# Kernel optimization log

Hardware: AMD Instinct MI355X
Metric: run time of the kernel (lower is better)

Reference implementation:

```python
import jax, jax.numpy as jnp
import numpy as np

N_NODES = 100000
D_IN = 128
D_OUT = 128
N_EDGES = 1600000
BN_EPS = 1e-5


def _glorot(key, fan_in, fan_out):
    limit = np.sqrt(6.0 / (fan_in + fan_out))
    return jax.random.uniform(key, (fan_in, fan_out), jnp.float32, -limit, limit)


def setup_inputs() -> dict:
    key = jax.random.key(0)
    k_x, k_e, k0, k1, k2 = jax.random.split(key, 5)
    x = jax.random.normal(k_x, (N_NODES, D_IN), jnp.float32)
    edge_index = jax.random.randint(k_e, (2, N_EDGES), 0, N_NODES, jnp.int64)
    return {
        "x": x,
        "edge_index": edge_index,
        "kernel": _glorot(k0, D_IN, D_OUT),
        "kernel1": _glorot(k1, D_IN, D_IN),
        "kernel2": _glorot(k2, D_IN, D_IN),
        "gamma": jnp.ones((D_IN,), jnp.float32),
        "beta": jnp.zeros((D_IN,), jnp.float32),
    }


def reference(x, edge_index, kernel, kernel1, kernel2, gamma, beta):
    N = x.shape[0]
    # BatchNorm1d (training mode: batch statistics, biased variance)
    mean = jnp.mean(x, axis=0)
    var = jnp.var(x, axis=0)
    xn = (x - mean) * jax.lax.rsqrt(var + BN_EPS) * gamma + beta

    mapped = xn @ kernel                                  # [N, D_OUT]
    s1 = jnp.tanh(jnp.sum((xn @ kernel1) * xn, axis=1))   # [N]
    s2 = jnp.tanh(jnp.sum((xn @ kernel2) * xn, axis=1))   # [N]

    src, dst = edge_index[0], edge_index[1]
    # edge score: adj values are 1 -> leaky_relu(s1[i] + s2[j]) for edge (i,j)
    e = jax.nn.leaky_relu(s1[src] + s2[dst], negative_slope=0.01)  # [E]

    # sparse row-wise softmax over dim 1 (segment softmax over src)
    emax = jax.ops.segment_max(e, src, num_segments=N)
    emax = jnp.where(jnp.isfinite(emax), emax, 0.0)
    ee = jnp.exp(e - emax[src])
    denom = jax.ops.segment_sum(ee, src, num_segments=N)
    attn = ee / jnp.maximum(denom[src], 1e-16)            # [E]

    # attention_adj @ mapped_inputs (scatter-add over src rows)
    out = jax.ops.segment_sum(attn[:, None] * mapped[dst], src, num_segments=N)
    return jax.nn.relu(out)
```

## Files before the change

kernel.cpp:

```cpp
#include <hip/hip_runtime.h>
#include <math.h>

#define N_NODES 100000
#define D 128
#define N_EDGES 1600000
#define BN_EPS 1e-5f
#define SCAN_NB 200
#define SCAN_BC 500
#define EG_BLOCKS 1563
#define EH_BLOCKS 782
#define GEMM_BLOCKS 1563

typedef __attribute__((ext_vector_type(8))) short bf16x8;
typedef __attribute__((ext_vector_type(4))) float f32x4;

__device__ inline unsigned short f2bf(float f) {
    unsigned int u = __float_as_uint(f);
    unsigned int r = u + 0x7FFFu + ((u >> 16) & 1u);
    return (unsigned short)(r >> 16);
}
__device__ inline float bf2f(unsigned short b) {
    return __uint_as_float(((unsigned int)b) << 16);
}

__global__ __launch_bounds__(256)
void stats_hist(const float* __restrict__ x, float* __restrict__ sums,
                const int* __restrict__ src, int* __restrict__ cnt,
                int* __restrict__ rank) {
    if (blockIdx.x < 256) {
        const int col  = threadIdx.x & 127;
        const int half = threadIdx.x >> 7;
        float s = 0.f, sq = 0.f;
        for (int r = blockIdx.x * 2 + half; r < N_NODES; r += 512) {
            float v = x[(size_t)r * D + col];
            s += v; sq += v * v;
        }
        __shared__ float ls[2][128];
        __shared__ float lq[2][128];
        ls[half][col] = s; lq[half][col] = sq;
        __syncthreads();
        if (threadIdx.x < 128) {
            atomicAdd(&sums[col],       ls[0][col] + ls[1][col]);
            atomicAdd(&sums[128 + col], lq[0][col] + lq[1][col]);
        }
    } else {
        const int b = blockIdx.x - 256;
        int* c = cnt + (size_t)(b & 7) * N_NODES;
        const int base = b * 2048 + threadIdx.x;
        if (b < EH_BLOCKS - 1) {
            int s[8];
#pragma unroll
            for (int j = 0; j < 8; ++j) s[j] = src[base + j * 256];
            int r[8];
#pragma unroll
            for (int j = 0; j < 8; ++j) r[j] = atomicAdd(&c[s[j]], 1);
#pragma unroll
            for (int j = 0; j < 8; ++j) rank[base + j * 256] = r[j];
        } else {
#pragma unroll
            for (int j = 0; j < 8; ++j) {
                int i = base + j * 256;
                if (i < N_EDGES) rank[i] = atomicAdd(&c[src[i]], 1);
            }
        }
    }
}

__global__ __launch_bounds__(256)
void finalize_pack(const float* __restrict__ sums, const float* __restrict__ gamma,
                   const float* __restrict__ beta, float* __restrict__ scale,
                   float* __restrict__ bias,
                   const float* __restrict__ k0, const float* __restrict__ k1,
                   const float* __restrict__ k2, unsigned short* __restrict__ wpack) {
    if (blockIdx.x == 0) {
        if (threadIdx.x < 128) {
            int c = threadIdx.x;
            float mean = sums[c] * (1.0f / N_NODES);
            float var  = sums[128 + c] * (1.0f / N_NODES) - mean * mean;
            float rstd = rsqrtf(var + BN_EPS);
            float sc = gamma[c] * rstd;
            scale[c] = sc;
            bias[c]  = beta[c] - mean * sc;
        }
        return;
    }
    int idx = (blockIdx.x - 1) * 256 + threadIdx.x;
    if (idx >= 3 * 4 * 8 * 64) return;
    int m    = idx >> 11;
    int r    = idx & 2047;
    int kk   = r >> 9;
    int r2   = r & 511;
    int nt   = r2 >> 6;
    int lane = r2 & 63;
    const float* W = (m == 0) ? k0 : (m == 1) ? k1 : k2;
    int col   = nt * 16 + (lane & 15);
    int kbase = kk * 32 + (lane >> 4) * 8;
    unsigned int wh[4], wl[4];
#pragma unroll
    for (int i = 0; i < 4; ++i) {
        float a = W[(kbase + 2 * i)     * 128 + col];
        float b = W[(kbase + 2 * i + 1) * 128 + col];
        unsigned short ah = f2bf(a), bh = f2bf(b);
        unsigned short al = f2bf(a - bf2f(ah)), bl = f2bf(b - bf2f(bh));
        wh[i] = (unsigned int)ah | ((unsigned int)bh << 16);
        wl[i] = (unsigned int)al | ((unsigned int)bl << 16);
    }
    uint4* outp = (uint4*)wpack;
    outp[idx]        = make_uint4(wh[0], wh[1], wh[2], wh[3]);
    outp[6144 + idx] = make_uint4(wl[0], wl[1], wl[2], wl[3]);
}

__global__ __launch_bounds__(256)
void scan_blocksum(const int* __restrict__ cnt, int* __restrict__ bsum) {
    __shared__ int red[256];
    const int b = blockIdx.x, t = threadIdx.x;
    const int base = b * SCAN_BC;
    int s = 0;
    for (int i = t; i < SCAN_BC; i += 256) {
        int node = base + i;
#pragma unroll
        for (int x = 0; x < 8; ++x) s += cnt[(size_t)x * N_NODES + node];
    }
    red[t] = s;
    __syncthreads();
    for (int off = 128; off; off >>= 1) {
        if (t < off) red[t] += red[t + off];
        __syncthreads();
    }
    if (t == 0) bsum[b] = red[0];
}

__global__ __launch_bounds__(256)
void scan_bases(int* __restrict__ bsum, int* __restrict__ row_off) {
    __shared__ int v[256];
    const int t = threadIdx.x;
    v[t] = (t < SCAN_NB) ? bsum[t] : 0;
    __syncthreads();
    for (int off = 1; off < 256; off <<= 1) {
        int u = (t >= off) ? v[t - off] : 0;
        __syncthreads();
        v[t] += u;
        __syncthreads();
    }
    if (t < SCAN_NB) bsum[t] = (t == 0) ? 0 : v[t - 1];
    if (t == 0) row_off[N_NODES] = v[SCAN_NB - 1];
}

__global__ __launch_bounds__(256)
void scan_write(int* __restrict__ cnt, const int* __restrict__ bsum,
                int* __restrict__ row_off) {
    __shared__ int tsum[256];
    const int b = blockIdx.x, t = threadIdx.x;
    const int i0 = b * SCAN_BC + t * 2;
    int c0[8], c1[8];
    int tot0 = 0, tot1 = 0;
    if (t < 250) {
#pragma unroll
        for (int x = 0; x < 8; ++x) {
            c0[x] = cnt[(size_t)x * N_NODES + i0];
            c1[x] = cnt[(size_t)x * N_NODES + i0 + 1];
            tot0 += c0[x]; tot1 += c1[x];
        }
    }
    tsum[t] = tot0 + tot1;
    __syncthreads();
    for (int off = 1; off < 256; off <<= 1) {
        int u = (t >= off) ? tsum[t - off] : 0;
        __syncthreads();
        tsum[t] += u;
        __syncthreads();
    }
    if (t < 250) {
        int run = bsum[b] + ((t == 0) ? 0 : tsum[t - 1]);
        row_off[i0] = run;
        int acc = run;
#pragma unroll
        for (int x = 0; x < 8; ++x) { cnt[(size_t)x * N_NODES + i0] = acc; acc += c0[x]; }
        run += tot0;
        row_off[i0 + 1] = run;
        acc = run;
#pragma unroll
        for (int x = 0; x < 8; ++x) { cnt[(size_t)x * N_NODES + i0 + 1] = acc; acc += c1[x]; }
    }
}

__global__ __launch_bounds__(256, 4)
void gemm_scatter(const float* __restrict__ x, const unsigned short* __restrict__ wpack,
                  const float* __restrict__ scale, const float* __restrict__ bias,
                  unsigned short* __restrict__ mapped, float* __restrict__ s1,
                  float* __restrict__ s2,
                  const int* __restrict__ src, const int* __restrict__ dst,
                  const int* __restrict__ cnt, const int* __restrict__ rank,
                  int* __restrict__ dst_sorted) {
    __shared__ unsigned short xbuf[64 * 128];
    if (blockIdx.x >= GEMM_BLOCKS) {
        const int b = blockIdx.x - GEMM_BLOCKS;
        const int* c = cnt + (size_t)((b >> 1) & 7) * N_NODES;
        const int base = b * 1024 + threadIdx.x;
#pragma unroll
        for (int k = 0; k < 4; ++k) {
            int i = base + k * 256;
            if (i < N_EDGES) dst_sorted[c[src[i]] + rank[i]] = dst[i];
        }
        return;
    }
    const int tid  = threadIdx.x;
    const int wave = tid >> 6, lane = tid & 63;
    const int base = blockIdx.x * 64;
    char* xb = (char*)xbuf;

    float2 sc = ((const float2*)scale)[lane];
    float2 bs = ((const float2*)bias)[lane];

    unsigned int hipack[16];
#pragma unroll
    for (int rr = 0; rr < 16; ++rr) {
        int row  = wave * 16 + rr;
        int node = base + row;
        float2 v = make_float2(0.f, 0.f);
        if (node < N_NODES) v = ((const float2*)x)[(size_t)node * 64 + lane];
        float f0 = v.x * sc.x + bs.x;
        float f1 = v.y * sc.y + bs.y;
        unsigned short h0 = f2bf(f0), h1 = f2bf(f1);
        unsigned short l0 = f2bf(f0 - bf2f(h0)), l1 = f2bf(f1 - bf2f(h1));
        hipack[rr] = (unsigned int)h0 | ((unsigned int)h1 << 16);
        int byte = (row * 256 + lane * 4) ^ ((row & 7) << 4);
        *(unsigned int*)(xb + byte) = (unsigned int)l0 | ((unsigned int)l1 << 16);
    }
    __syncthreads();

    const int arow  = wave * 16 + (lane & 15);
    const int lrow0 = wave * 16 + (lane >> 4) * 4;

    bf16x8 al[4];
#pragma unroll
    for (int kk = 0; kk < 4; ++kk) {
        int byte = (arow * 256 + kk * 64 + (lane >> 4) * 16) ^ ((arow & 7) << 4);
        al[kk] = *(const bf16x8*)(xb + byte);
    }
    unsigned int xlo[16];
#pragma unroll
    for (int nt = 0; nt < 8; ++nt) {
#pragma unroll
        for (int reg = 0; reg < 4; ++reg) {
            int lrow = lrow0 + reg;
            int col  = nt * 16 + (lane & 15);
            int byte = (lrow * 256 + col * 2) ^ ((lrow & 7) << 4);
            unsigned short v = *(const unsigned short*)(xb + byte);
            int idx = nt * 4 + reg;
            if (idx & 1) xlo[idx >> 1] |= ((unsigned int)v) << 16;
            else         xlo[idx >> 1]  = v;
        }
    }
    __syncthreads();

#pragma unroll
    for (int rr = 0; rr < 16; ++rr) {
        int row  = wave * 16 + rr;
        int byte = (row * 256 + lane * 4) ^ ((row & 7) << 4);
        *(unsigned int*)(xb + byte) = hipack[rr];
    }
    __syncthreads();

    bf16x8 ah[4];
#pragma unroll
    for (int kk = 0; kk < 4; ++kk) {
        int byte = (arow * 256 + kk * 64 + (lane >> 4) * 16) ^ ((arow & 7) << 4);
        ah[kk] = *(const bf16x8*)(xb + byte);
    }

    const bf16x8* wp = (const bf16x8*)wpack;

    {
        f32x4 acc[8] = {};
#pragma unroll
        for (int kk = 0; kk < 4; ++kk) {
#pragma unroll
            for (int nt = 0; nt < 8; ++nt) {
                bf16x8 b = wp[(kk * 8 + nt) * 64 + lane];
                acc[nt] = __builtin_amdgcn_mfma_f32_16x16x32_bf16(ah[kk], b, acc[nt], 0, 0, 0);
            }
        }
        int crow = base + wave * 16 + (lane >> 4) * 4;
        int ccol = lane & 15;
#pragma unroll
        for (int nt = 0; nt < 8; ++nt) {
#pragma unroll
            for (int reg = 0; reg < 4; ++reg) {
                int node = crow + reg;
                if (node < N_NODES)
                    mapped[(size_t)node * 128 + nt * 16 + ccol] = f2bf(acc[nt][reg]);
            }
        }
    }

    {
        float p1[4] = {0.f, 0.f, 0.f, 0.f};
        float p2[4] = {0.f, 0.f, 0.f, 0.f};
#pragma unroll
        for (int nt = 0; nt < 8; ++nt) {
            f32x4 a1 = {0.f, 0.f, 0.f, 0.f};
            f32x4 a2 = {0.f, 0.f, 0.f, 0.f};
#pragma unroll
            for (int kk = 0; kk < 4; ++kk) {
                int fi = (kk * 8 + nt) * 64 + lane;
                bf16x8 b1h = wp[2048 * 1 + fi];
                bf16x8 b1l = wp[6144 + 2048 * 1 + fi];
                bf16x8 b2h = wp[2048 * 2 + fi];
                bf16x8 b2l = wp[6144 + 2048 * 2 + fi];
                a1 = __builtin_amdgcn_mfma_f32_16x16x32_bf16(ah[kk], b1h, a1, 0, 0, 0);
                a1 = __builtin_amdgcn_mfma_f32_16x16x32_bf16(al[kk], b1h, a1, 0, 0, 0);
                a1 = __builtin_amdgcn_mfma_f32_16x16x32_bf16(ah[kk], b1l, a1, 0, 0, 0);
                a2 = __builtin_amdgcn_mfma_f32_16x16x32_bf16(ah[kk], b2h, a2, 0, 0, 0);
                a2 = __builtin_amdgcn_mfma_f32_16x16x32_bf16(al[kk], b2h, a2, 0, 0, 0);
                a2 = __builtin_amdgcn_mfma_f32_16x16x32_bf16(ah[kk], b2l, a2, 0, 0, 0);
            }
            int col = nt * 16 + (lane & 15);
#pragma unroll
            for (int reg = 0; reg < 4; ++reg) {
                int lrow = lrow0 + reg;
                int byte = (lrow * 256 + col * 2) ^ ((lrow & 7) << 4);
                float xh = bf2f(*(const unsigned short*)(xb + byte));
                int idx = nt * 4 + reg;
                unsigned short lo16 = (idx & 1) ? (unsigned short)(xlo[idx >> 1] >> 16)
                                                : (unsigned short)(xlo[idx >> 1] & 0xFFFFu);
                float xv = xh + bf2f(lo16);
                p1[reg] = fmaf(a1[reg], xv, p1[reg]);
                p2[reg] = fmaf(a2[reg], xv, p2[reg]);
            }
        }
#pragma unroll
        for (int reg = 0; reg < 4; ++reg) {
#pragma unroll
            for (int off = 1; off < 16; off <<= 1) {
                p1[reg] += __shfl_xor(p1[reg], off);
                p2[reg] += __shfl_xor(p2[reg], off);
            }
        }
        if ((lane & 15) == 0) {
            int nbase = base + wave * 16 + (lane >> 4) * 4;
#pragma unroll
            for (int reg = 0; reg < 4; ++reg) {
                int node = nbase + reg;
                if (node < N_NODES) {
                    s1[node] = tanhf(p1[reg]);
                    s2[node] = tanhf(p2[reg]);
                }
            }
        }
    }
}

__global__ __launch_bounds__(256)
void node_aggregate(const int* __restrict__ row_off, const int* __restrict__ dst_sorted,
                    const float* __restrict__ s1, const float* __restrict__ s2,
                    const unsigned int* __restrict__ mapped,
                    float* __restrict__ out) {
    const int wave = threadIdx.x >> 6, lane = threadIdx.x & 63;
    const int n = blockIdx.x * 4 + wave;
    if (n >= N_NODES) return;
    const int beg = row_off[n], end = row_off[n + 1];
    const int deg = end - beg;
    float acc0 = 0.f, acc1 = 0.f, den = 0.f;

#define GATHER8(WSRC, DSRC, J)                                                   \
    {                                                                            \
        float w0 = __shfl(WSRC, (J) + 0), w1 = __shfl(WSRC, (J) + 1);            \
        float w2 = __shfl(WSRC, (J) + 2), w3 = __shfl(WSRC, (J) + 3);            \
        float w4 = __shfl(WSRC, (J) + 4), w5 = __shfl(WSRC, (J) + 5);            \
        float w6 = __shfl(WSRC, (J) + 6), w7 = __shfl(WSRC, (J) + 7);            \
        int d0 = __shfl(DSRC, (J) + 0), d1 = __shfl(DSRC, (J) + 1);              \
        int d2 = __shfl(DSRC, (J) + 2), d3 = __shfl(DSRC, (J) + 3);              \
        int d4 = __shfl(DSRC, (J) + 4), d5 = __shfl(DSRC, (J) + 5);              \
        int d6 = __shfl(DSRC, (J) + 6), d7 = __shfl(DSRC, (J) + 7);              \
        unsigned int m0 = mapped[(size_t)d0 * 64 + lane];                        \
        unsigned int m1 = mapped[(size_t)d1 * 64 + lane];                        \
        unsigned int m2 = mapped[(size_t)d2 * 64 + lane];                        \
        unsigned int m3 = mapped[(size_t)d3 * 64 + lane];                        \
        unsigned int m4 = mapped[(size_t)d4 * 64 + lane];                        \
        unsigned int m5 = mapped[(size_t)d5 * 64 + lane];                        \
        unsigned int m6 = mapped[(size_t)d6 * 64 + lane];                        \
        unsigned int m7 = mapped[(size_t)d7 * 64 + lane];                        \
        acc0 = fmaf(w0, bf2f((unsigned short)(m0 & 0xFFFFu)), acc0);             \
        acc1 = fmaf(w0, bf2f((unsigned short)(m0 >> 16)), acc1);                 \
        acc0 = fmaf(w1, bf2f((unsigned short)(m1 & 0xFFFFu)), acc0);             \
        acc1 = fmaf(w1, bf2f((unsigned short)(m1 >> 16)), acc1);                 \
        acc0 = fmaf(w2, bf2f((unsigned short)(m2 & 0xFFFFu)), acc0);             \
        acc1 = fmaf(w2, bf2f((unsigned short)(m2 >> 16)), acc1);                 \
        acc0 = fmaf(w3, bf2f((unsigned short)(m3 & 0xFFFFu)), acc0);             \
        acc1 = fmaf(w3, bf2f((unsigned short)(m3 >> 16)), acc1);                 \
        acc0 = fmaf(w4, bf2f((unsigned short)(m4 & 0xFFFFu)), acc0);             \
        acc1 = fmaf(w4, bf2f((unsigned short)(m4 >> 16)), acc1);                 \
        acc0 = fmaf(w5, bf2f((unsigned short)(m5 & 0xFFFFu)), acc0);             \
        acc1 = fmaf(w5, bf2f((unsigned short)(m5 >> 16)), acc1);                 \
        acc0 = fmaf(w6, bf2f((unsigned short)(m6 & 0xFFFFu)), acc0);             \
        acc1 = fmaf(w6, bf2f((unsigned short)(m6 >> 16)), acc1);                 \
        acc0 = fmaf(w7, bf2f((unsigned short)(m7 & 0xFFFFu)), acc0);             \
        acc1 = fmaf(w7, bf2f((unsigned short)(m7 >> 16)), acc1);                 \
    }

    if (deg > 0 && deg <= 64) {
        float s1n = s1[n];
        int   d_l = 0; float e_l = -INFINITY;
        if (lane < deg) {
            d_l = dst_sorted[beg + lane];
            float v = s1n + s2[d_l];
            e_l = v > 0.f ? v : 0.01f * v;
        }
        float m = e_l;
#pragma unroll
        for (int off = 1; off < 64; off <<= 1) m = fmaxf(m, __shfl_xor(m, off));
        float w_l = (lane < deg) ? expf(e_l - m) : 0.f;
        den = w_l;
        int j = 0;
        for (; j + 8 <= deg; j += 8) GATHER8(w_l, d_l, j)
        for (; j < deg; ++j) {
            float wj = __shfl(w_l, j);
            int   dj = __shfl(d_l, j);
            unsigned int mv = mapped[(size_t)dj * 64 + lane];
            acc0 = fmaf(wj, bf2f((unsigned short)(mv & 0xFFFFu)), acc0);
            acc1 = fmaf(wj, bf2f((unsigned short)(mv >> 16)), acc1);
        }
    } else if (deg > 64) {
        float s1n = s1[n];
        float m = -INFINITY;
        for (int chunk = beg; chunk < end; chunk += 64) {
            if (chunk + lane < end) {
                int dj = dst_sorted[chunk + lane];
                float v = s1n + s2[dj];
                m = fmaxf(m, v > 0.f ? v : 0.01f * v);
            }
        }
#pragma unroll
        for (int off = 1; off < 64; off <<= 1) m = fmaxf(m, __shfl_xor(m, off));
        for (int chunk = beg; chunk < end; chunk += 64) {
            int nc = min(64, end - chunk);
            int   d_l = 0; float w_l = 0.f;
            if (lane < nc) {
                d_l = dst_sorted[chunk + lane];
                float v = s1n + s2[d_l];
                float e = v > 0.f ? v : 0.01f * v;
                w_l = expf(e - m);
            }
            den += w_l;
            int j = 0;
            for (; j + 8 <= nc; j += 8) GATHER8(w_l, d_l, j)
            for (; j < nc; ++j) {
                float wj = __shfl(w_l, j);
                int   dj = __shfl(d_l, j);
                unsigned int mv = mapped[(size_t)dj * 64 + lane];
                acc0 = fmaf(wj, bf2f((unsigned short)(mv & 0xFFFFu)), acc0);
                acc1 = fmaf(wj, bf2f((unsigned short)(mv >> 16)), acc1);
            }
        }
    }
#undef GATHER8

    if (deg > 0) {
#pragma unroll
        for (int off = 1; off < 64; off <<= 1) den += __shfl_xor(den, off);
        float inv = 1.f / fmaxf(den, 1e-16f);
        acc0 *= inv; acc1 *= inv;
    }
    ((float2*)out)[(size_t)n * 64 + lane] = make_float2(fmaxf(acc0, 0.f), fmaxf(acc1, 0.f));
}

extern "C" void kernel_launch(void* const* d_in, const int* in_sizes, int n_in,
                              void* d_out, int out_size, void* d_ws, size_t ws_size,
                              hipStream_t stream) {
    const float* x     = (const float*)d_in[0];
    const int*   ei    = (const int*)d_in[1];
    const float* k0    = (const float*)d_in[2];
    const float* k1    = (const float*)d_in[3];
    const float* k2    = (const float*)d_in[4];
    const float* gamma = (const float*)d_in[5];
    const float* beta  = (const float*)d_in[6];
    float* out = (float*)d_out;

    const int* src = ei;
    const int* dst = ei + N_EDGES;

    char* ws = (char*)d_ws;
    unsigned short* wpack = (unsigned short*)ws;           ws += 6 * 128 * 128 * 2;
    float* s1       = (float*)ws;                          ws += N_NODES * 4;
    float* s2       = (float*)ws;                          ws += N_NODES * 4;
    float* scale    = (float*)ws;                          ws += 128 * 4;
    float* bias     = (float*)ws;                          ws += 128 * 4;
    float* sums     = (float*)ws;                          ws += 256 * 4;
    int*   bsum     = (int*)ws;                            ws += 256 * 4;
    int*   row_off  = (int*)ws;                            ws += (N_NODES + 1) * 4;
    int*   cnt      = (int*)ws;                            ws += (size_t)8 * N_NODES * 4;
    int*   rank     = (int*)ws;                            ws += (size_t)N_EDGES * 4;
    int*   dst_sorted = (int*)ws;                          ws += (size_t)N_EDGES * 4;
    unsigned short* mapped = (unsigned short*)ws;          ws += (size_t)N_NODES * D * 2;

    hipMemsetAsync(sums, 0, 256 * sizeof(float), stream);
    hipMemsetAsync(cnt, 0, (size_t)8 * N_NODES * sizeof(int), stream);

    stats_hist<<<256 + EH_BLOCKS, 256, 0, stream>>>(x, sums, src, cnt, rank);
    finalize_pack<<<25, 256, 0, stream>>>(sums, gamma, beta, scale, bias,
                                          k0, k1, k2, wpack);
    scan_blocksum<<<SCAN_NB, 256, 0, stream>>>(cnt, bsum);
    scan_bases<<<1, 256, 0, stream>>>(bsum, row_off);
    scan_write<<<SCAN_NB, 256, 0, stream>>>(cnt, bsum, row_off);
    gemm_scatter<<<GEMM_BLOCKS + EG_BLOCKS, 256, 0, stream>>>(
        x, wpack, scale, bias, mapped, s1, s2, src, dst, cnt, rank, dst_sorted);
    node_aggregate<<<(N_NODES + 3) / 4, 256, 0, stream>>>(row_off, dst_sorted,
                                                          s1, s2,
                                                          (const unsigned int*)mapped,
                                                          out);
}
```

Before: 308.2 us.

## Spread edge histogram across stats, pack and GEMM launches; widen gather unroll

The src-degree histogram windows are split across three kernels (stats, finalize_pack, and the GEMM launch) so the atomic histogram work overlaps with BN statistics, weight packing and the dense GEMM, instead of mostly running alongside the stats pass. The edge scatter into dst_sorted moves out of the GEMM launch into its own kernel after the scan, which adds a launch but leaves the GEMM kernel free to host histogram blocks. Separately, node_aggregate gathers 16 neighbour rows per batch before falling back to 8, to keep more loads in flight. The risks are the extra launch, register pressure from the wider gather, and an unbalanced split that leaves one kernel as the bottleneck.

```diff
diff --git a/kernel.cpp b/kernel.cpp
--- a/kernel.cpp
+++ b/kernel.cpp
@@ -9,6 +9,9 @@
 #define SCAN_BC 500
 #define EG_BLOCKS 1563
 #define EH_BLOCKS 782
+#define H1 156
+#define H2 16
+#define H3 (EH_BLOCKS - H1 - H2)
 #define GEMM_BLOCKS 1563
 
 typedef __attribute__((ext_vector_type(8))) short bf16x8;
@@ -21,6 +24,28 @@
 }
 __device__ inline float bf2f(unsigned short b) {
     return __uint_as_float(((unsigned int)b) << 16);
+}
+
+__device__ inline void hist_window(int w, const int* __restrict__ src,
+                                   int* __restrict__ cnt, int* __restrict__ rank) {
+    int* c = cnt + (size_t)(w & 7) * N_NODES;
+    const int base = w * 2048 + threadIdx.x;
+    if (w < EH_BLOCKS - 1) {
+        int s[8];
+#pragma unroll
+        for (int j = 0; j < 8; ++j) s[j] = src[base + j * 256];
+        int r[8];
+#pragma unroll
+        for (int j = 0; j < 8; ++j) r[j] = atomicAdd(&c[s[j]], 1);
+#pragma unroll
+        for (int j = 0; j < 8; ++j) rank[base + j * 256] = r[j];
+    } else {
+#pragma unroll
+        for (int j = 0; j < 8; ++j) {
+            int i = base + j * 256;
+            if (i < N_EDGES) rank[i] = atomicAdd(&c[src[i]], 1);
+        }
+    }
 }
 
 __global__ __launch_bounds__(256)
@@ -44,25 +69,7 @@
             atomicAdd(&sums[128 + col], lq[0][col] + lq[1][col]);
         }
     } else {
-        const int b = blockIdx.x - 256;
-        int* c = cnt + (size_t)(b & 7) * N_NODES;
-        const int base = b * 2048 + threadIdx.x;
-        if (b < EH_BLOCKS - 1) {
-            int s[8];
-#pragma unroll
-            for (int j = 0; j < 8; ++j) s[j] = src[base + j * 256];
-            int r[8];
-#pragma unroll
-            for (int j = 0; j < 8; ++j) r[j] = atomicAdd(&c[s[j]], 1);
-#pragma unroll
-            for (int j = 0; j < 8; ++j) rank[base + j * 256] = r[j];
-        } else {
-#pragma unroll
-            for (int j = 0; j < 8; ++j) {
-                int i = base + j * 256;
-                if (i < N_EDGES) rank[i] = atomicAdd(&c[src[i]], 1);
-            }
-        }
+        hist_window(blockIdx.x - 256, src, cnt, rank);
     }
 }
 
@@ -71,7 +78,13 @@
                    const float* __restrict__ beta, float* __restrict__ scale,
                    float* __restrict__ bias,
                    const float* __restrict__ k0, const float* __restrict__ k1,
-                   const float* __restrict__ k2, unsigned short* __restrict__ wpack) {
+                   const float* __restrict__ k2, unsigned short* __restrict__ wpack,
+                   const int* __restrict__ src, int* __restrict__ cnt,
+                   int* __restrict__ rank) {
+    if (blockIdx.x >= 25) {
+        hist_window(H1 + (blockIdx.x - 25), src, cnt, rank);
+        return;
+    }
     if (blockIdx.x == 0) {
         if (threadIdx.x < 128) {
             int c = threadIdx.x;
@@ -110,98 +123,16 @@
     outp[6144 + idx] = make_uint4(wl[0], wl[1], wl[2], wl[3]);
 }
 
-__global__ __launch_bounds__(256)
-void scan_blocksum(const int* __restrict__ cnt, int* __restrict__ bsum) {
-    __shared__ int red[256];
-    const int b = blockIdx.x, t = threadIdx.x;
-    const int base = b * SCAN_BC;
-    int s = 0;
-    for (int i = t; i < SCAN_BC; i += 256) {
-        int node = base + i;
-#pragma unroll
-        for (int x = 0; x < 8; ++x) s += cnt[(size_t)x * N_NODES + node];
-    }
-    red[t] = s;
-    __syncthreads();
-    for (int off = 128; off; off >>= 1) {
-        if (t < off) red[t] += red[t + off];
-        __syncthreads();
-    }
-    if (t == 0) bsum[b] = red[0];
-}
-
-__global__ __launch_bounds__(256)
-void scan_bases(int* __restrict__ bsum, int* __restrict__ row_off) {
-    __shared__ int v[256];
-    const int t = threadIdx.x;
-    v[t] = (t < SCAN_NB) ? bsum[t] : 0;
-    __syncthreads();
-    for (int off = 1; off < 256; off <<= 1) {
-        int u = (t >= off) ? v[t - off] : 0;
-        __syncthreads();
-        v[t] += u;
-        __syncthreads();
-    }
-    if (t < SCAN_NB) bsum[t] = (t == 0) ? 0 : v[t - 1];
-    if (t == 0) row_off[N_NODES] = v[SCAN_NB - 1];
-}
-
-__global__ __launch_bounds__(256)
-void scan_write(int* __restrict__ cnt, const int* __restrict__ bsum,
-                int* __restrict__ row_off) {
-    __shared__ int tsum[256];
-    const int b = blockIdx.x, t = threadIdx.x;
-    const int i0 = b * SCAN_BC + t * 2;
-    int c0[8], c1[8];
-    int tot0 = 0, tot1 = 0;
-    if (t < 250) {
-#pragma unroll
-        for (int x = 0; x < 8; ++x) {
-            c0[x] = cnt[(size_t)x * N_NODES + i0];
-            c1[x] = cnt[(size_t)x * N_NODES + i0 + 1];
-            tot0 += c0[x]; tot1 += c1[x];
-        }
-    }
-    tsum[t] = tot0 + tot1;
-    __syncthreads();
-    for (int off = 1; off < 256; off <<= 1) {
-        int u = (t >= off) ? tsum[t - off] : 0;
-        __syncthreads();
-        tsum[t] += u;
-        __syncthreads();
-    }
-    if (t < 250) {
-        int run = bsum[b] + ((t == 0) ? 0 : tsum[t - 1]);
-        row_off[i0] = run;
-        int acc = run;
-#pragma unroll
-        for (int x = 0; x < 8; ++x) { cnt[(size_t)x * N_NODES + i0] = acc; acc += c0[x]; }
-        run += tot0;
-        row_off[i0 + 1] = run;
-        acc = run;
-#pragma unroll
-        for (int x = 0; x < 8; ++x) { cnt[(size_t)x * N_NODES + i0 + 1] = acc; acc += c1[x]; }
-    }
-}
-
 __global__ __launch_bounds__(256, 4)
-void gemm_scatter(const float* __restrict__ x, const unsigned short* __restrict__ wpack,
-                  const float* __restrict__ scale, const float* __restrict__ bias,
-                  unsigned short* __restrict__ mapped, float* __restrict__ s1,
-                  float* __restrict__ s2,
-                  const int* __restrict__ src, const int* __restrict__ dst,
-                  const int* __restrict__ cnt, const int* __restrict__ rank,
-                  int* __restrict__ dst_sorted) {
+void gemm_hist(const float* __restrict__ x, const unsigned short* __restrict__ wpack,
+               const float* __restrict__ scale, const float* __restrict__ bias,
+               unsigned short* __restrict__ mapped, float* __restrict__ s1,
+               float* __restrict__ s2,
+               const int* __restrict__ src, int* __restrict__ cnt,
+               int* __restrict__ rank) {
     __shared__ unsigned short xbuf[64 * 128];
     if (blockIdx.x >= GEMM_BLOCKS) {
-        const int b = blockIdx.x - GEMM_BLOCKS;
-        const int* c = cnt + (size_t)((b >> 1) & 7) * N_NODES;
-        const int base = b * 1024 + threadIdx.x;
-#pragma unroll
-        for (int k = 0; k < 4; ++k) {
-            int i = base + k * 256;
-            if (i < N_EDGES) dst_sorted[c[src[i]] + rank[i]] = dst[i];
-        }
+        hist_window(H1 + H2 + (blockIdx.x - GEMM_BLOCKS), src, cnt, rank);
         return;
     }
     const int tid  = threadIdx.x;
@@ -352,6 +283,94 @@
 }
 
 __global__ __launch_bounds__(256)
+void scan_blocksum(const int* __restrict__ cnt, int* __restrict__ bsum) {
+    __shared__ int red[256];
+    const int b = blockIdx.x, t = threadIdx.x;
+    const int base = b * SCAN_BC;
+    int s = 0;
+    for (int i = t; i < SCAN_BC; i += 256) {
+        int node = base + i;
+#pragma unroll
+        for (int x = 0; x < 8; ++x) s += cnt[(size_t)x * N_NODES + node];
+    }
+    red[t] = s;
+    __syncthreads();
+    for (int off = 128; off; off >>= 1) {
+        if (t < off) red[t] += red[t + off];
+        __syncthreads();
+    }
+    if (t == 0) bsum[b] = red[0];
+}
+
+__global__ __launch_bounds__(256)
+void scan_bases(int* __restrict__ bsum, int* __restrict__ row_off) {
+    __shared__ int v[256];
+    const int t = threadIdx.x;
+    v[t] = (t < SCAN_NB) ? bsum[t] : 0;
+    __syncthreads();
+    for (int off = 1; off < 256; off <<= 1) {
+        int u = (t >= off) ? v[t - off] : 0;
+        __syncthreads();
+        v[t] += u;
+        __syncthreads();
+    }
+    if (t < SCAN_NB) bsum[t] = (t == 0) ? 0 : v[t - 1];
+    if (t == 0) row_off[N_NODES] = v[SCAN_NB - 1];
+}
+
+__global__ __launch_bounds__(256)
+void scan_write(int* __restrict__ cnt, const int* __restrict__ bsum,
+                int* __restrict__ row_off) {
+    __shared__ int tsum[256];
+    const int b = blockIdx.x, t = threadIdx.x;
+    const int i0 = b * SCAN_BC + t * 2;
+    int c0[8], c1[8];
+    int tot0 = 0, tot1 = 0;
+    if (t < 250) {
+#pragma unroll
+        for (int x = 0; x < 8; ++x) {
+            c0[x] = cnt[(size_t)x * N_NODES + i0];
+            c1[x] = cnt[(size_t)x * N_NODES + i0 + 1];
+            tot0 += c0[x]; tot1 += c1[x];
+        }
+    }
+    tsum[t] = tot0 + tot1;
+    __syncthreads();
+    for (int off = 1; off < 256; off <<= 1) {
+        int u = (t >= off) ? tsum[t - off] : 0;
+        __syncthreads();
+        tsum[t] += u;
+        __syncthreads();
+    }
+    if (t < 250) {
+        int run = bsum[b] + ((t == 0) ? 0 : tsum[t - 1]);
+        row_off[i0] = run;
+        int acc = run;
+#pragma unroll
+        for (int x = 0; x < 8; ++x) { cnt[(size_t)x * N_NODES + i0] = acc; acc += c0[x]; }
+        run += tot0;
+        row_off[i0 + 1] = run;
+        acc = run;
+#pragma unroll
+        for (int x = 0; x < 8; ++x) { cnt[(size_t)x * N_NODES + i0 + 1] = acc; acc += c1[x]; }
+    }
+}
+
+__global__ __launch_bounds__(256)
+void scatter_edges(const int* __restrict__ src, const int* __restrict__ dst,
+                   const int* __restrict__ cnt, const int* __restrict__ rank,
+                   int* __restrict__ dst_sorted) {
+    const int b = blockIdx.x;
+    const int* c = cnt + (size_t)((b >> 1) & 7) * N_NODES;
+    const int base = b * 1024 + threadIdx.x;
+#pragma unroll
+    for (int k = 0; k < 4; ++k) {
+        int i = base + k * 256;
+        if (i < N_EDGES) dst_sorted[c[src[i]] + rank[i]] = dst[i];
+    }
+}
+
+__global__ __launch_bounds__(256)
 void node_aggregate(const int* __restrict__ row_off, const int* __restrict__ dst_sorted,
                     const float* __restrict__ s1, const float* __restrict__ s2,
                     const unsigned int* __restrict__ mapped,
@@ -363,40 +382,22 @@
     const int deg = end - beg;
     float acc0 = 0.f, acc1 = 0.f, den = 0.f;
 
-#define GATHER8(WSRC, DSRC, J)                                                   \
+#define GATHER_N(NN, WSRC, DSRC, J)                                              \
     {                                                                            \
-        float w0 = __shfl(WSRC, (J) + 0), w1 = __shfl(WSRC, (J) + 1);            \
-        float w2 = __shfl(WSRC, (J) + 2), w3 = __shfl(WSRC, (J) + 3);            \
-        float w4 = __shfl(WSRC, (J) + 4), w5 = __shfl(WSRC, (J) + 5);            \
-        float w6 = __shfl(WSRC, (J) + 6), w7 = __shfl(WSRC, (J) + 7);            \
-        int d0 = __shfl(DSRC, (J) + 0), d1 = __shfl(DSRC, (J) + 1);              \
-        int d2 = __shfl(DSRC, (J) + 2), d3 = __shfl(DSRC, (J) + 3);              \
-        int d4 = __shfl(DSRC, (J) + 4), d5 = __shfl(DSRC, (J) + 5);              \
-        int d6 = __shfl(DSRC, (J) + 6), d7 = __shfl(DSRC, (J) + 7);              \
-        unsigned int m0 = mapped[(size_t)d0 * 64 + lane];                        \
-        unsigned int m1 = mapped[(size_t)d1 * 64 + lane];                        \
-        unsigned int m2 = mapped[(size_t)d2 * 64 + lane];                        \
-        unsigned int m3 = mapped[(size_t)d3 * 64 + lane];                        \
-        unsigned int m4 = mapped[(size_t)d4 * 64 + lane];                        \
-        unsigned int m5 = mapped[(size_t)d5 * 64 + lane];                        \
-        unsigned int m6 = mapped[(size_t)d6 * 64 + lane];                        \
-        unsigned int m7 = mapped[(size_t)d7 * 64 + lane];                        \
-        acc0 = fmaf(w0, bf2f((unsigned short)(m0 & 0xFFFFu)), acc0);             \
-        acc1 = fmaf(w0, bf2f((unsigned short)(m0 >> 16)), acc1);                 \
-        acc0 = fmaf(w1, bf2f((unsigned short)(m1 & 0xFFFFu)), acc0);             \
-        acc1 = fmaf(w1, bf2f((unsigned short)(m1 >> 16)), acc1);                 \
-        acc0 = fmaf(w2, bf2f((unsigned short)(m2 & 0xFFFFu)), acc0);             \
-        acc1 = fmaf(w2, bf2f((unsigned short)(m2 >> 16)), acc1);                 \
-        acc0 = fmaf(w3, bf2f((unsigned short)(m3 & 0xFFFFu)), acc0);             \
-        acc1 = fmaf(w3, bf2f((unsigned short)(m3 >> 16)), acc1);                 \
-        acc0 = fmaf(w4, bf2f((unsigned short)(m4 & 0xFFFFu)), acc0);             \
-        acc1 = fmaf(w4, bf2f((unsigned short)(m4 >> 16)), acc1);                 \
-        acc0 = fmaf(w5, bf2f((unsigned short)(m5 & 0xFFFFu)), acc0);             \
-        acc1 = fmaf(w5, bf2f((unsigned short)(m5 >> 16)), acc1);                 \
-        acc0 = fmaf(w6, bf2f((unsigned short)(m6 & 0xFFFFu)), acc0);             \
-        acc1 = fmaf(w6, bf2f((unsigned short)(m6 >> 16)), acc1);                 \
-        acc0 = fmaf(w7, bf2f((unsigned short)(m7 & 0xFFFFu)), acc0);             \
-        acc1 = fmaf(w7, bf2f((unsigned short)(m7 >> 16)), acc1);                 \
+        float w_[NN]; int dd_[NN]; unsigned int mm_[NN];                         \
+_Pragma("unroll")                                                                \
+        for (int q = 0; q < NN; ++q) {                                           \
+            w_[q] = __shfl(WSRC, (J) + q);                                       \
+            dd_[q] = __shfl(DSRC, (J) + q);                                      \
+        }                                                                        \
+_Pragma("unroll")                                                                \
+        for (int q = 0; q < NN; ++q)                                             \
+            mm_[q] = mapped[(size_t)dd_[q] * 64 + lane];                         \
+_Pragma("unroll")                                                                \
+        for (int q = 0; q < NN; ++q) {                                           \
+            acc0 = fmaf(w_[q], bf2f((unsigned short)(mm_[q] & 0xFFFFu)), acc0);  \
+            acc1 = fmaf(w_[q], bf2f((unsigned short)(mm_[q] >> 16)), acc1);      \
+        }                                                                        \
     }
 
     if (deg > 0 && deg <= 64) {
@@ -413,7 +414,8 @@
         float w_l = (lane < deg) ? expf(e_l - m) : 0.f;
         den = w_l;
         int j = 0;
-        for (; j + 8 <= deg; j += 8) GATHER8(w_l, d_l, j)
+        for (; j + 16 <= deg; j += 16) GATHER_N(16, w_l, d_l, j)
+        for (; j + 8 <= deg; j += 8)   GATHER_N(8, w_l, d_l, j)
         for (; j < deg; ++j) {
             float wj = __shfl(w_l, j);
             int   dj = __shfl(d_l, j);
@@ -444,7 +446,8 @@
             }
             den += w_l;
             int j = 0;
-            for (; j + 8 <= nc; j += 8) GATHER8(w_l, d_l, j)
+            for (; j + 16 <= nc; j += 16) GATHER_N(16, w_l, d_l, j)
+            for (; j + 8 <= nc; j += 8)   GATHER_N(8, w_l, d_l, j)
             for (; j < nc; ++j) {
                 float wj = __shfl(w_l, j);
                 int   dj = __shfl(d_l, j);
@@ -454,7 +457,7 @@
             }
         }
     }
-#undef GATHER8
+#undef GATHER_N
 
     if (deg > 0) {
 #pragma unroll
@@ -497,14 +500,15 @@
     hipMemsetAsync(sums, 0, 256 * sizeof(float), stream);
     hipMemsetAsync(cnt, 0, (size_t)8 * N_NODES * sizeof(int), stream);
 
-    stats_hist<<<256 + EH_BLOCKS, 256, 0, stream>>>(x, sums, src, cnt, rank);
-    finalize_pack<<<25, 256, 0, stream>>>(sums, gamma, beta, scale, bias,
-                                          k0, k1, k2, wpack);
+    stats_hist<<<256 + H1, 256, 0, stream>>>(x, sums, src, cnt, rank);
+    finalize_pack<<<25 + H2, 256, 0, stream>>>(sums, gamma, beta, scale, bias,
+                                               k0, k1, k2, wpack, src, cnt, rank);
+    gemm_hist<<<GEMM_BLOCKS + H3, 256, 0, stream>>>(x, wpack, scale, bias,
+                                                    mapped, s1, s2, src, cnt, rank);
     scan_blocksum<<<SCAN_NB, 256, 0, stream>>>(cnt, bsum);
     scan_bases<<<1, 256, 0, stream>>>(bsum, row_off);
     scan_write<<<SCAN_NB, 256, 0, stream>>>(cnt, bsum, row_off);
-    gemm_scatter<<<GEMM_BLOCKS + EG_BLOCKS, 256, 0, stream>>>(
-        x, wpack, scale, bias, mapped, s1, s2, src, dst, cnt, rank, dst_sorted);
+    scatter_edges<<<EG_BLOCKS, 256, 0, stream>>>(src, dst, cnt, rank, dst_sorted);
     node_aggregate<<<(N_NODES + 3) / 4, 256, 0, stream>>>(row_off, dst_sorted,
                                                           s1, s2,
                                                           (const unsigned int*)mapped,
```

Measured after the change: 330.5 us. +7.3%, slower.
